# Kernel tuning notes

Measured on AMD Instinct MI355X. Metric: run time of the kernel, lower is better.

Reference implementation:

```python
import jax, jax.numpy as jnp
import numpy as np

TAU = 0.5
EPS_NORM = 1e-12  # torch F.normalize eps
EPS_DEN = 1e-8


def setup_inputs() -> dict:
    key = jax.random.key(0)
    k1, k2 = jax.random.split(key)
    N, D = 16384, 128
    z1 = jax.random.normal(k1, (N, D), dtype=jnp.float32)
    z2 = jax.random.normal(k2, (N, D), dtype=jnp.float32)
    return {"z1": z1, "z2": z2}


def _l2norm(x):
    # torch F.normalize: x / max(||x||, eps)
    n = jnp.sqrt(jnp.sum(x * x, axis=-1, keepdims=True))
    return x / jnp.maximum(n, EPS_NORM)


def reference(z1, z2):
    z1n = _l2norm(z1)
    z2n = _l2norm(z2)
    # cosine similarity of unit vectors == dot product -> single GEMM [N, N]
    sim = jnp.exp(jnp.einsum('id,jd->ij', z1n, z2n) / TAU)
    pos = jnp.exp(jnp.sum(z1n * z2n, axis=-1) / TAU)  # diagonal positives [N]
    denom = jnp.sum(sim, axis=1) + EPS_DEN
    loss = -jnp.mean(jnp.log(pos / denom))
    return loss
```

## Files before the change

### kernel.cpp

```cpp
#include <hip/hip_runtime.h>
#include <hip/hip_bf16.h>
#include <hip/hip_fp8.h>


#define N_ROWS 16384
#define DIM 128
#define JSPLIT 16
#define COLS_PER_BLOCK (N_ROWS / JSPLIT)
#define JCHUNK 32
#define NCHUNK (COLS_PER_BLOCK / JCHUNK)
#define ROWS_PER_BLOCK 256
#define ITILES (N_ROWS / ROWS_PER_BLOCK)
#define GRID_TOTAL (ITILES * JSPLIT)

#define SCALE 2.8853900817779268f

typedef __attribute__((ext_vector_type(8))) int   int8v;
typedef __attribute__((ext_vector_type(4))) int   int4v;
typedef __attribute__((ext_vector_type(4))) float floatx4;

#if __has_builtin(__builtin_amdgcn_exp2f)
#define EXP2(x) __builtin_amdgcn_exp2f(x)
#else
#define EXP2(x) exp2f(x)
#endif

__device__ inline floatx4 mfma_fp8_k128(int8v a, int8v b, floatx4 c) {
  return __builtin_amdgcn_mfma_scale_f32_16x16x128_f8f6f4(
      a, b, c, 0, 0, 0, 0x7F7F7F7F, 0, 0x7F7F7F7F);
}

__device__ inline void gload_lds16(const void* gptr, void* lptr) {
  __builtin_amdgcn_global_load_lds(
      (const __attribute__((address_space(1))) void*)gptr,
      (__attribute__((address_space(3))) void*)lptr, 16, 0, 0);
}

__device__ inline short pack_fp8x2(float x, float y) {
#if __has_builtin(__builtin_amdgcn_cvt_pk_fp8_f32)
  int p = __builtin_amdgcn_cvt_pk_fp8_f32(x, y, 0, false);
  return (short)(p & 0xFFFF);
#else
  __hip_fp8_e4m3 a(x), b(y);
  return (short)((unsigned char)a.__x | ((unsigned short)(unsigned char)b.__x << 8));
#endif
}

__global__ __launch_bounds__(256) void norm_kernel(
    const float* __restrict__ z1, const float* __restrict__ z2,
    unsigned char* __restrict__ z1q, unsigned char* __restrict__ z2q,
    float* __restrict__ diag, float* __restrict__ denom,
    float* __restrict__ out) {
  int tid = threadIdx.x;
  int wave = tid >> 6, lane = tid & 63;
  int row = blockIdx.x * 4 + wave;
  const float2* p1 = (const float2*)(z1 + (size_t)row * DIM);
  const float2* p2 = (const float2*)(z2 + (size_t)row * DIM);
  float2 a = p1[lane], b = p2[lane];
  float s11 = a.x * a.x + a.y * a.y;
  float s22 = b.x * b.x + b.y * b.y;
  float s12 = a.x * b.x + a.y * b.y;
#pragma unroll
  for (int m = 32; m >= 1; m >>= 1) {
    s11 += __shfl_xor(s11, m);
    s22 += __shfl_xor(s22, m);
    s12 += __shfl_xor(s12, m);
  }
  float inv1 = 1.0f / fmaxf(sqrtf(s11), 1e-12f);
  float inv2 = 1.0f / fmaxf(sqrtf(s22), 1e-12f);
  float sc1 = inv1 * SCALE;
  ((short*)(z1q + (size_t)row * DIM))[lane] = pack_fp8x2(a.x * sc1, a.y * sc1);
  ((short*)(z2q + (size_t)row * DIM))[lane] = pack_fp8x2(b.x * inv2, b.y * inv2);
  if (lane == 0) {
    diag[row]  = s12 * inv1 * inv2;
    denom[row] = 0.0f;
  }
  if (blockIdx.x == 0 && tid == 0) out[0] = 0.0f;
}

__global__ __launch_bounds__(256, 4) void sim_kernel(
    const unsigned char* __restrict__ z1q,
    const unsigned char* __restrict__ z2q,
    float* __restrict__ denom) {
  __shared__ int4v lds[2][JCHUNK * 8];

  int tid = threadIdx.x;
  int w   = tid >> 6;
  int q   = (tid >> 4) & 3;
  int l15 = tid & 15;
  int s   = l15 & 7;
  int itile  = blockIdx.x & (ITILES - 1);
  int jsplit = blockIdx.x >> 6;
  int i0 = itile * ROWS_PER_BLOCK + w * 64;

  const floatx4 ZERO4 = {0.f, 0.f, 0.f, 0.f};

  int8v afrag0, afrag1, afrag2, afrag3;
#define LOAD_AFRAG(dst, ii)                                                  \
  do {                                                                       \
    const int4v* rp =                                                        \
        (const int4v*)(z1q + (size_t)(i0 + (ii) * 16 + l15) * DIM);          \
    int4v a0 = rp[q * 2], a1 = rp[q * 2 + 1];                                \
    int8v af;                                                                \
    af[0] = a0[0]; af[1] = a0[1]; af[2] = a0[2]; af[3] = a0[3];              \
    af[4] = a1[0]; af[5] = a1[1]; af[6] = a1[2]; af[7] = a1[3];              \
    dst = af;                                                                \
  } while (0)
  LOAD_AFRAG(afrag0, 0);
  LOAD_AFRAG(afrag1, 1);
  LOAD_AFRAG(afrag2, 2);
  LOAD_AFRAG(afrag3, 3);

  floatx4 rowsum0 = ZERO4, rowsum1 = ZERO4, rowsum2 = ZERO4, rowsum3 = ZERO4;
  floatx4 pacc0 = {-1e30f, -1e30f, -1e30f, -1e30f};
  floatx4 pacc1 = {-1e30f, -1e30f, -1e30f, -1e30f};
  floatx4 pacc2 = {-1e30f, -1e30f, -1e30f, -1e30f};
  floatx4 pacc3 = {-1e30f, -1e30f, -1e30f, -1e30f};

  const char* Bbase = (const char*)z2q + (size_t)jsplit * COLS_PER_BLOCK * DIM;

#define STAGE(cidx, bufi)                                                    \
  do {                                                                       \
    const char* _ck = Bbase + (size_t)(cidx) * JCHUNK * DIM;                 \
    char* _dst = (char*)&lds[bufi][0];                                       \
    int _row = tid >> 3, _gl = tid & 7;                                      \
    int _u = _gl ^ (_row & 7);                                               \
    int _o = 2 * (_u & 3) + (_u >> 2);                                       \
    gload_lds16(_ck + (size_t)_row * DIM + _o * 16,                          \
                _dst + (size_t)tid * 16);                                    \
  } while (0)

  STAGE(0, 0);
  __syncthreads();

  int lo_i = q ^ s;
  int hi_i = lo_i ^ 4;

#define MFMA_FLUSH(af, pacc, rowsum)                                         \
  do {                                                                       \
    floatx4 nacc = mfma_fp8_k128(af, bf, ZERO4);                             \
    floatx4 e;                                                               \
    _Pragma("unroll")                                                        \
    for (int r = 0; r < 4; ++r) e[r] = EXP2(pacc[r]);                        \
    rowsum += e;                                                             \
    pacc = nacc;                                                             \
  } while (0)

#pragma unroll 1
  for (int c = 0; c < NCHUNK; ++c) {
    if (c + 1 < NCHUNK) STAGE(c + 1, (c + 1) & 1);
    const int4v* buf = &lds[c & 1][0];

#pragma unroll
    for (int jj = 0; jj < 2; ++jj) {
      int rbase = (jj * 16 + l15) * 8;
      int4v lo = buf[rbase + lo_i];
      int4v hi = buf[rbase + hi_i];
      int8v bf;
      bf[0] = lo[0]; bf[1] = lo[1]; bf[2] = lo[2]; bf[3] = lo[3];
      bf[4] = hi[0]; bf[5] = hi[1]; bf[6] = hi[2]; bf[7] = hi[3];

      MFMA_FLUSH(afrag0, pacc0, rowsum0);
      MFMA_FLUSH(afrag1, pacc1, rowsum1);
      MFMA_FLUSH(afrag2, pacc2, rowsum2);
      MFMA_FLUSH(afrag3, pacc3, rowsum3);
    }
    __syncthreads();
  }
  {
    floatx4 e;
#pragma unroll
    for (int r = 0; r < 4; ++r) e[r] = EXP2(pacc0[r]);
    rowsum0 += e;
#pragma unroll
    for (int r = 0; r < 4; ++r) e[r] = EXP2(pacc1[r]);
    rowsum1 += e;
#pragma unroll
    for (int r = 0; r < 4; ++r) e[r] = EXP2(pacc2[r]);
    rowsum2 += e;
#pragma unroll
    for (int r = 0; r < 4; ++r) e[r] = EXP2(pacc3[r]);
    rowsum3 += e;
  }

#define COMMIT(rowsum, ii)                                                   \
  do {                                                                       \
    _Pragma("unroll")                                                        \
    for (int r = 0; r < 4; ++r) {                                            \
      float v = rowsum[r];                                                   \
      v += __shfl_xor(v, 1);                                                 \
      v += __shfl_xor(v, 2);                                                 \
      v += __shfl_xor(v, 4);                                                 \
      v += __shfl_xor(v, 8);                                                 \
      if (l15 == 0) atomicAdd(&denom[i0 + (ii) * 16 + q * 4 + r], v);        \
    }                                                                        \
  } while (0)
  COMMIT(rowsum0, 0);
  COMMIT(rowsum1, 1);
  COMMIT(rowsum2, 2);
  COMMIT(rowsum3, 3);
}

__global__ __launch_bounds__(256) void loss_kernel(
    const float* __restrict__ denom, const float* __restrict__ diag,
    float* __restrict__ out) {
  int row = blockIdx.x * 256 + threadIdx.x;
  float t = 2.0f * diag[row] - __logf(denom[row] + 1e-8f);
#pragma unroll
  for (int m = 32; m >= 1; m >>= 1) t += __shfl_xor(t, m);
  if ((threadIdx.x & 63) == 0) atomicAdd(out, -t * (1.0f / N_ROWS));
}

extern "C" void kernel_launch(void* const* d_in, const int* in_sizes, int n_in,
                              void* d_out, int out_size, void* d_ws, size_t ws_size,
                              hipStream_t stream) {
  const float* z1 = (const float*)d_in[0];
  const float* z2 = (const float*)d_in[1];
  char* ws = (char*)d_ws;
  unsigned char* z1q = (unsigned char*)ws;
  unsigned char* z2q = (unsigned char*)(ws + (size_t)N_ROWS * DIM);
  float* denom = (float*)(ws + (size_t)2 * N_ROWS * DIM);
  float* diag  = (float*)(ws + (size_t)2 * N_ROWS * DIM + (size_t)N_ROWS * 4);
  float* outp  = (float*)d_out;

  norm_kernel<<<N_ROWS / 4, 256, 0, stream>>>(z1, z2, z1q, z2q, diag, denom, outp);
  sim_kernel<<<GRID_TOTAL, 256, 0, stream>>>(z1q, z2q, denom);
  loss_kernel<<<N_ROWS / 256, 256, 0, stream>>>(denom, diag, outp);
}
```

Measured before the change: 109.7 us.

## Give each wave private LDS double buffers and drop block barriers

```diff
diff --git a/kernel.cpp b/kernel.cpp
--- a/kernel.cpp
+++ b/kernel.cpp
@@ -12,6 +12,8 @@
 #define ROWS_PER_BLOCK 256
 #define ITILES (N_ROWS / ROWS_PER_BLOCK)
 #define GRID_TOTAL (ITILES * JSPLIT)
+#define CHUNK_BYTES (JCHUNK * DIM)
+#define BUF_BYTES (JCHUNK * 8 * 16)
 
 #define SCALE 2.8853900817779268f
 
@@ -82,13 +84,14 @@
     const unsigned char* __restrict__ z1q,
     const unsigned char* __restrict__ z2q,
     float* __restrict__ denom) {
-  __shared__ int4v lds[2][JCHUNK * 8];
+  __shared__ int4v lds[4][2][JCHUNK * 8];
 
   int tid = threadIdx.x;
-  int w   = tid >> 6;
-  int q   = (tid >> 4) & 3;
-  int l15 = tid & 15;
-  int s   = l15 & 7;
+  int w    = tid >> 6;
+  int lane = tid & 63;
+  int q    = (lane >> 4) & 3;
+  int l15  = lane & 15;
+  int s    = l15 & 7;
   int itile  = blockIdx.x & (ITILES - 1);
   int jsplit = blockIdx.x >> 6;
   int i0 = itile * ROWS_PER_BLOCK + w * 64;
@@ -119,19 +122,21 @@
 
   const char* Bbase = (const char*)z2q + (size_t)jsplit * COLS_PER_BLOCK * DIM;
 
+  int _r0 = lane >> 3, _gl = lane & 7;
+  int _u = _gl ^ _r0;
+  int _o = 2 * (_u & 3) + (_u >> 2);
+  const char* gsrc = Bbase + (size_t)_r0 * DIM + _o * 16;
+  char* ldst = (char*)&lds[w][0][0] + (size_t)lane * 16;
+
 #define STAGE(cidx, bufi)                                                    \
   do {                                                                       \
-    const char* _ck = Bbase + (size_t)(cidx) * JCHUNK * DIM;                 \
-    char* _dst = (char*)&lds[bufi][0];                                       \
-    int _row = tid >> 3, _gl = tid & 7;                                      \
-    int _u = _gl ^ (_row & 7);                                               \
-    int _o = 2 * (_u & 3) + (_u >> 2);                                       \
-    gload_lds16(_ck + (size_t)_row * DIM + _o * 16,                          \
-                _dst + (size_t)tid * 16);                                    \
-  } while (0)
-
-  STAGE(0, 0);
-  __syncthreads();
+    const char* _src = gsrc + (size_t)(cidx) * CHUNK_BYTES;                  \
+    char* _d = ldst + (size_t)(bufi) * BUF_BYTES;                            \
+    gload_lds16(_src + 0 * (8 * DIM), _d + 0 * 1024);                        \
+    gload_lds16(_src + 1 * (8 * DIM), _d + 1 * 1024);                        \
+    gload_lds16(_src + 2 * (8 * DIM), _d + 2 * 1024);                        \
+    gload_lds16(_src + 3 * (8 * DIM), _d + 3 * 1024);                        \
+  } while (0)
 
   int lo_i = q ^ s;
   int hi_i = lo_i ^ 4;
@@ -146,10 +151,16 @@
     pacc = nacc;                                                             \
   } while (0)
 
+  STAGE(0, 0);
 #pragma unroll 1
   for (int c = 0; c < NCHUNK; ++c) {
-    if (c + 1 < NCHUNK) STAGE(c + 1, (c + 1) & 1);
-    const int4v* buf = &lds[c & 1][0];
+    if (c + 1 < NCHUNK) {
+      STAGE(c + 1, (c + 1) & 1);
+      asm volatile("s_waitcnt vmcnt(4)" ::: "memory");
+    } else {
+      asm volatile("s_waitcnt vmcnt(0)" ::: "memory");
+    }
+    const int4v* buf = &lds[w][c & 1][0];
 
 #pragma unroll
     for (int jj = 0; jj < 2; ++jj) {
@@ -165,7 +176,6 @@
       MFMA_FLUSH(afrag2, pacc2, rowsum2);
       MFMA_FLUSH(afrag3, pacc3, rowsum3);
     }
-    __syncthreads();
   }
   {
     floatx4 e;
```

Result: no change. 111.6 us (+1.8%).
